# Performance work log

Measured on AMD Instinct MI355X. Metric: run time of the kernel, lower is better.

## Reference

```python
import jax, jax.numpy as jnp
import numpy as np

EPS = 1e-6
WINDOW = 1024  # config.sliding_window; mask: causal AND (q_idx - kv_idx < WINDOW)


def rms_norm(x, w=None):
    y = x * jax.lax.rsqrt(jnp.mean(jnp.square(x), axis=-1, keepdims=True) + EPS)
    return y * w if w is not None else y


def rotate_half(x):
    x1, x2 = jnp.split(x, 2, axis=-1)
    return jnp.concatenate([-x2, x1], axis=-1)


def apply_rope(x, cos, sin):
    # x: [B,S,H,D], cos/sin: [B,S,D] -> unsqueeze head dim (rotary_dim == D, x_pass empty)
    cos = cos[:, :, None, :]
    sin = sin[:, :, None, :]
    return x * cos + rotate_half(x) * sin


def setup_inputs() -> dict:
    key = jax.random.key(0)
    ks = jax.random.split(key, 8)
    B, S, HID, NH, NKV, D = 1, 2048, 2560, 8, 4, 256
    scale = 0.02
    hidden_states = jax.random.normal(ks[0], (B, S, HID), dtype=jnp.float32)
    wq = jax.random.normal(ks[1], (HID, NH * D), dtype=jnp.float32) * scale
    wk = jax.random.normal(ks[2], (HID, NKV * D), dtype=jnp.float32) * scale
    wv = jax.random.normal(ks[3], (HID, NKV * D), dtype=jnp.float32) * scale
    wo = jax.random.normal(ks[4], (NH * D, HID), dtype=jnp.float32) * scale
    q_norm_w = jnp.ones((D,), dtype=jnp.float32)
    k_norm_w = jnp.ones((D,), dtype=jnp.float32)
    # standard RoPE tables, rotary_dim = head_dim
    pos = jnp.arange(S, dtype=jnp.float32)
    inv_freq = 1.0 / (10000.0 ** (jnp.arange(0, D, 2, dtype=jnp.float32) / D))
    freqs = pos[:, None] * inv_freq[None, :]           # [S, D/2]
    emb = jnp.concatenate([freqs, freqs], axis=-1)     # [S, D]
    cos = jnp.cos(emb)[None]                           # [1, S, D]
    sin = jnp.sin(emb)[None]
    return dict(hidden_states=hidden_states, cos=cos, sin=sin,
                wq=wq, wk=wk, wv=wv, wo=wo,
                q_norm_w=q_norm_w, k_norm_w=k_norm_w)


def reference(hidden_states, cos, sin, wq, wk, wv, wo, q_norm_w, k_norm_w):
    B, S, _ = hidden_states.shape
    D = q_norm_w.shape[0]
    # projections -> [B,S,H,D]
    q = (hidden_states @ wq).reshape(B, S, -1, D)
    k = (hidden_states @ wk).reshape(B, S, -1, D)
    v = (hidden_states @ wv).reshape(B, S, -1, D)
    # QK-norm then RoPE (v gets non-affine RMSNorm)
    q = apply_rope(rms_norm(q, q_norm_w), cos, sin)
    k = apply_rope(rms_norm(k, k_norm_w), cos, sin)
    v = rms_norm(v)
    NH, NKV = q.shape[2], k.shape[2]
    rep = NH // NKV  # GQA: repeat KV heads
    k = jnp.repeat(k, rep, axis=2)
    v = jnp.repeat(v, rep, axis=2)
    # attention with scale=1.0 (QK-norm replaces 1/sqrt(d))
    scores = jnp.einsum('bqhd,bkhd->bhqk', q, k)
    qi = jnp.arange(S)[:, None]
    ki = jnp.arange(S)[None, :]
    mask = (ki <= qi) & (qi - ki < WINDOW)  # causal sliding window
    scores = jnp.where(mask[None, None], scores, -jnp.inf)
    attn = jax.nn.softmax(scores, axis=-1)
    out = jnp.einsum('bhqk,bkhd->bqhd', attn, v).reshape(B, S, -1)
    return out @ wo
```

## Files before the change

### kernel.cpp

```cpp
#include <hip/hip_runtime.h>
#include <hip/hip_bf16.h>
#include <math.h>

#define S_LEN 2048
#define HID 2560
#define NH 8
#define NKV 4
#define HD 256
#define WINDOW 1024

typedef short short8 __attribute__((ext_vector_type(8)));
typedef short short4_t __attribute__((ext_vector_type(4)));
typedef float f32x4 __attribute__((ext_vector_type(4)));
typedef float float4_t __attribute__((ext_vector_type(4)));

__device__ __forceinline__ short bf16_rne(float x) {
  unsigned u = __float_as_uint(x);
  return (short)((u + 0x7FFFu + ((u >> 16) & 1u)) >> 16);
}
__device__ __forceinline__ void split2(float x, short &h, short &l) {
  unsigned u = __float_as_uint(x);
  unsigned hb = (u + 0x7FFFu + ((u >> 16) & 1u)) & 0xFFFF0000u;
  h = (short)(hb >> 16);
  float r = x - __uint_as_float(hb);
  l = bf16_rne(r);
}

__device__ __forceinline__ void gload16(const short* g, short* l) {
  __builtin_amdgcn_global_load_lds(
      (const __attribute__((address_space(1))) void*)g,
      (__attribute__((address_space(3))) void*)l, 16, 0, 0);
}

#define SWZ(g, r) ((((g) ^ ((r) & 7))) * 8)
template <int MODE>
__device__ __forceinline__ void gemm_body(
    const short* __restrict__ Ah, const short* __restrict__ Al,
    const short* __restrict__ Bh, const short* __restrict__ Bl,
    float* __restrict__ C, int K, int ldc, int m0, int n0, int tid,
    short (*__restrict__ Ahs)[64], short (*__restrict__ Als)[64],
    short (*__restrict__ Bhs)[64], short (*__restrict__ Bls)[64]) {
  constexpr bool USE_AL = (MODE & 1) != 0;
  constexpr bool USE_BL = (MODE & 2) != 0;
  const int wv = tid >> 6, lane = tid & 63;
  const int wm = (wv >> 1) * 32, wn = (wv & 1) * 64;
  const int quad = lane >> 4, col = lane & 15;
  const int lr = lane >> 3;
  const size_t lgofs = (size_t)(((lane & 7) ^ lr)) * 8;
  const size_t aBase = (size_t)(m0 + lr) * K + lgofs;
  const size_t bBase = (size_t)(n0 + lr) * K + lgofs;

  f32x4 acc[2][4];
#pragma unroll
  for (int i = 0; i < 2; i++)
#pragma unroll
    for (int j = 0; j < 4; j++) acc[i][j] = (f32x4){0.f, 0.f, 0.f, 0.f};

  for (int k0 = 0; k0 < K; k0 += 64) {
#pragma unroll
    for (int c = wv; c < 8; c += 4) {
      const size_t go = aBase + (size_t)c * 8 * K + k0;
      gload16(Ah + go, &Ahs[c * 8][0]);
      if (USE_AL) gload16(Al + go, &Als[c * 8][0]);
    }
#pragma unroll
    for (int c = wv; c < 16; c += 4) {
      const size_t go = bBase + (size_t)c * 8 * K + k0;
      gload16(Bh + go, &Bhs[c * 8][0]);
      if (USE_BL) gload16(Bl + go, &Bls[c * 8][0]);
    }
    __syncthreads();
#pragma unroll
    for (int ks = 0; ks < 2; ks++) {
      const int g = ks * 4 + quad;
      short8 afh[2], afl[2], bfh[4], bfl[4];
#pragma unroll
      for (int i = 0; i < 2; i++) {
        int ar = wm + i * 16 + col;
        afh[i] = *reinterpret_cast<const short8*>(&Ahs[ar][SWZ(g, ar)]);
        if (USE_AL)
          afl[i] = *reinterpret_cast<const short8*>(&Als[ar][SWZ(g, ar)]);
      }
#pragma unroll
      for (int j = 0; j < 4; j++) {
        int br = wn + j * 16 + col;
        bfh[j] = *reinterpret_cast<const short8*>(&Bhs[br][SWZ(g, br)]);
        if (USE_BL)
          bfl[j] = *reinterpret_cast<const short8*>(&Bls[br][SWZ(g, br)]);
      }
#pragma unroll
      for (int i = 0; i < 2; i++)
#pragma unroll
        for (int j = 0; j < 4; j++) {
          acc[i][j] = __builtin_amdgcn_mfma_f32_16x16x32_bf16(afh[i], bfh[j], acc[i][j], 0, 0, 0);
          if (USE_BL)
            acc[i][j] = __builtin_amdgcn_mfma_f32_16x16x32_bf16(afh[i], bfl[j], acc[i][j], 0, 0, 0);
          if (USE_AL)
            acc[i][j] = __builtin_amdgcn_mfma_f32_16x16x32_bf16(afl[i], bfh[j], acc[i][j], 0, 0, 0);
        }
    }
    __syncthreads();
  }
#pragma unroll
  for (int i = 0; i < 2; i++)
#pragma unroll
    for (int j = 0; j < 4; j++)
#pragma unroll
      for (int r = 0; r < 4; r++)
        C[(size_t)(m0 + wm + i * 16 + quad * 4 + r) * ldc + n0 + wn + j * 16 + col] =
            acc[i][j][r];
}

template <int MODE>
__global__ __launch_bounds__(256, 3)
void gemm_presplit(const short* __restrict__ Ah, const short* __restrict__ Al,
                   const short* __restrict__ Bh, const short* __restrict__ Bl,
                   float* __restrict__ C, int K, int ldc) {
  __shared__ short Ahs[64][64];
  __shared__ short Als[(MODE & 1) ? 64 : 1][64];
  __shared__ short Bhs[128][64];
  __shared__ short Bls[(MODE & 2) ? 128 : 1][64];
  gemm_body<MODE>(Ah, Al, Bh, Bl, C, K, ldc, blockIdx.y * 64, blockIdx.x * 128,
                  threadIdx.x, Ahs, Als, Bhs, Bls);
}

__global__ __launch_bounds__(256, 3)
void gemm_qkv(const short* __restrict__ Ah, const short* __restrict__ Al,
              const short* __restrict__ qkvTh, const short* __restrict__ qkvTl,
              float* __restrict__ Cqkv) {
  __shared__ short Ahs[64][64];
  __shared__ short Als[64][64];
  __shared__ short Bhs[128][64];
  __shared__ short Bls[128][64];
  const int b = blockIdx.x;
  if (b < 256) {
    gemm_body<2>(Ah, Al, qkvTh + (size_t)3072 * HID, qkvTl + (size_t)3072 * HID,
                 Cqkv + 3072, HID, 4096, (b / 8) * 64, (b % 8) * 128,
                 threadIdx.x, Ahs, Als, Bhs, Bls);
  } else {
    const int t = b - 256;
    gemm_body<3>(Ah, Al, qkvTh, qkvTl, Cqkv, HID, 4096, (t / 24) * 64,
                 (t % 24) * 128, threadIdx.x, Ahs, Als, Bhs, Bls);
  }
}

__device__ __forceinline__ void wsplitT_body(const float* __restrict__ W,
                                             short* __restrict__ WTh,
                                             short* __restrict__ WTl,
                                             int KW, int NW, int n_ofs,
                                             int k0, int n0, int tid,
                                             float (*T)[65]) {
  const int r = tid >> 4, c4 = (tid & 15) * 4;
#pragma unroll
  for (int p = 0; p < 4; p++) {
    float4_t v = *reinterpret_cast<const float4_t*>(
        &W[(size_t)(k0 + r + p * 16) * NW + n0 + c4]);
#pragma unroll
    for (int e = 0; e < 4; e++) T[r + p * 16][c4 + e] = v[e];
  }
  __syncthreads();
  const int gk = tid & 7;
#pragma unroll
  for (int pass = 0; pass < 2; pass++) {
    const int n_loc = (tid >> 3) + pass * 32;
    short8 hv, lv;
#pragma unroll
    for (int e = 0; e < 8; e++) {
      short hh, ll;
      split2(T[gk * 8 + e][n_loc], hh, ll);
      hv[e] = hh; lv[e] = ll;
    }
    size_t base = (size_t)(n_ofs + n0 + n_loc) * KW + k0 + gk * 8;
    *reinterpret_cast<short8*>(WTh + base) = hv;
    *reinterpret_cast<short8*>(WTl + base) = lv;
  }
}

__global__ __launch_bounds__(256)
void prep_kernel(const float* __restrict__ hs, const float* __restrict__ wq,
                 const float* __restrict__ wk, const float* __restrict__ wv,
                 const float* __restrict__ wo, short* __restrict__ Ah,
                 short* __restrict__ Al, short* __restrict__ qkvTh,
                 short* __restrict__ qkvTl, short* __restrict__ woTh,
                 short* __restrict__ woTl) {
  __shared__ float T[64][65];
  const int bx = blockIdx.x;
  const int tid = threadIdx.x;
  if (bx < 5120) {
    const int i = bx * 256 + tid;
    float4_t v = reinterpret_cast<const float4_t*>(hs)[i];
    short4_t h, l;
#pragma unroll
    for (int e = 0; e < 4; e++) {
      short hh, ll;
      split2(v[e], hh, ll);
      h[e] = hh; l[e] = ll;
    }
    reinterpret_cast<short4_t*>(Ah)[i] = h;
    reinterpret_cast<short4_t*>(Al)[i] = l;
  } else if (bx < 6400) {
    const int local = bx - 5120;
    wsplitT_body(wq, qkvTh, qkvTl, HID, 2048, 0, (local % 40) * 64,
                 (local / 40) * 64, tid, T);
  } else if (bx < 7040) {
    const int local = bx - 6400;
    wsplitT_body(wk, qkvTh, qkvTl, HID, 1024, 2048, (local % 40) * 64,
                 (local / 40) * 64, tid, T);
  } else if (bx < 7680) {
    const int local = bx - 7040;
    wsplitT_body(wv, qkvTh, qkvTl, HID, 1024, 3072, (local % 40) * 64,
                 (local / 40) * 64, tid, T);
  } else {
    const int local = bx - 7680;
    wsplitT_body(wo, woTh, woTl, 2048, HID, 0, (local % 32) * 64,
                 (local / 32) * 64, tid, T);
  }
}

__global__ __launch_bounds__(256)
void norm_kernel(const float* __restrict__ Cqkv, const float* __restrict__ kw,
                 const float* __restrict__ cosb, const float* __restrict__ sinb,
                 short* __restrict__ kh, short* __restrict__ kl,
                 short* __restrict__ vtb) {
  const int unit = blockIdx.x * 4 + (threadIdx.x >> 6);
  const int u = unit & 7;
  const int sq = unit >> 3;
  const int t = threadIdx.x & 63;
  const int d = t * 4;
  const int colbase = (u < 4) ? 2048 + u * HD : 3072 + (u - 4) * HD;
  const float4_t x = *reinterpret_cast<const float4_t*>(
      &Cqkv[(size_t)sq * 4096 + colbase + d]);
  float v = x[0] * x[0] + x[1] * x[1] + x[2] * x[2] + x[3] * x[3];
#pragma unroll
  for (int off = 32; off; off >>= 1) v += __shfl_xor(v, off);
  const float scale = rsqrtf(v * (1.0f / HD) + 1e-6f);
  if (u < 4) {
    const float4_t w = *reinterpret_cast<const float4_t*>(kw + d);
    const float4_t cb = *reinterpret_cast<const float4_t*>(
        &cosb[(size_t)sq * HD + d]);
    const float4_t sb = *reinterpret_cast<const float4_t*>(
        &sinb[(size_t)sq * HD + d]);
    const float sgn = (t < 32) ? -1.f : 1.f;
    short4_t hv, lv;
#pragma unroll
    for (int e = 0; e < 4; e++) {
      const float n = x[e] * scale * w[e];
      const float other = __shfl_xor(n, 32);
      const float r = n * cb[e] + sgn * other * sb[e];
      short hh, ll;
      split2(r, hh, ll);
      hv[e] = hh; lv[e] = ll;
    }
    const size_t b = ((size_t)sq * NKV + u) * HD + d;
    *reinterpret_cast<short4_t*>(kh + b) = hv;
    *reinterpret_cast<short4_t*>(kl + b) = lv;
  } else {
    const int hh = u - 4;
#pragma unroll
    for (int e = 0; e < 4; e++)
      vtb[((size_t)hh * HD + d + e) * S_LEN + sq] = bf16_rne(x[e] * scale);
  }
}

#define KSW(g, r) (((g) ^ ((r) & 7)) * 8)
#define VSW(g, d) ((((g) + ((d) >> 1)) & 3) * 8)
__global__ __launch_bounds__(256, 2)
void flash_attn2(const float* __restrict__ qn, int qrs,
                 const float* __restrict__ qw, const float* __restrict__ cosb,
                 const float* __restrict__ sinb,
                 const short* __restrict__ kh, const short* __restrict__ kl,
                 const short* __restrict__ vtb, float* __restrict__ oA,
                 float* __restrict__ oB, float* __restrict__ mlA,
                 float* __restrict__ mlB) {
  __shared__ short Kh[32][256], Kl[32][256];
  __shared__ short Vb[256][32];
  __shared__ short Ps[64][32];
  const int qt = blockIdx.x, h = blockIdx.y, sp = blockIdx.z;
  const int kvh = h >> 1;
  const int q0 = qt * 64;
  const int tid = threadIdx.x;
  const int w = tid >> 6, lane = tid & 63;
  const int quad = lane >> 4, col = lane & 15;
  float* oOut = sp ? oB : oA;
  float* mlOut = sp ? mlB : mlA;
  short8 qh[8], ql[8];
  {
    const int sq = q0 + w * 16 + col;
    const float* qrow = qn + (size_t)sq * qrs + h * HD;
    float xq[8][8];
    float ssum = 0.f;
#pragma unroll
    for (int s8 = 0; s8 < 8; s8++) {
      const int d0 = s8 * 32 + quad * 8;
      float4_t a = *reinterpret_cast<const float4_t*>(qrow + d0);
      float4_t b = *reinterpret_cast<const float4_t*>(qrow + d0 + 4);
#pragma unroll
      for (int e = 0; e < 4; e++) {
        xq[s8][e] = a[e];
        xq[s8][4 + e] = b[e];
        ssum += a[e] * a[e] + b[e] * b[e];
      }
    }
    ssum += __shfl_xor(ssum, 16);
    ssum += __shfl_xor(ssum, 32);
    const float scale = rsqrtf(ssum * (1.0f / HD) + 1e-6f);
#pragma unroll
    for (int s8 = 0; s8 < 8; s8++) {
      const int d0 = s8 * 32 + quad * 8;
      float4_t w0 = *reinterpret_cast<const float4_t*>(qw + d0);
      float4_t w1 = *reinterpret_cast<const float4_t*>(qw + d0 + 4);
#pragma unroll
      for (int e = 0; e < 4; e++) {
        xq[s8][e] *= scale * w0[e];
        xq[s8][4 + e] *= scale * w1[e];
      }
    }
    const float* crow = cosb + (size_t)sq * HD;
    const float* srow = sinb + (size_t)sq * HD;
#pragma unroll
    for (int s8 = 0; s8 < 8; s8++) {
      const int d0 = s8 * 32 + quad * 8;
      float4_t c0 = *reinterpret_cast<const float4_t*>(crow + d0);
      float4_t c1 = *reinterpret_cast<const float4_t*>(crow + d0 + 4);
      float4_t s0 = *reinterpret_cast<const float4_t*>(srow + d0);
      float4_t s1 = *reinterpret_cast<const float4_t*>(srow + d0 + 4);
      const float sgn = (s8 < 4) ? -1.f : 1.f;
      const int pp = s8 ^ 4;
#pragma unroll
      for (int e = 0; e < 4; e++) {
        short hh, ll;
        split2(xq[s8][e] * c0[e] + sgn * xq[pp][e] * s0[e], hh, ll);
        qh[s8][e] = hh; ql[s8][e] = ll;
        split2(xq[s8][4 + e] * c1[e] + sgn * xq[pp][4 + e] * s1[e], hh, ll);
        qh[s8][4 + e] = hh; ql[s8][4 + e] = ll;
      }
    }
  }
  f32x4 o[16];
#pragma unroll
  for (int i = 0; i < 16; i++) o[i] = (f32x4){0.f, 0.f, 0.f, 0.f};
  float m_r[4] = {-INFINITY, -INFINITY, -INFINITY, -INFINITY};
  float l_r[4] = {0.f, 0.f, 0.f, 0.f};
  const int lo_t = (q0 > 1023) ? ((q0 - 1023) >> 5) : 0;
  const int hi_t = (q0 + 63) >> 5;
  const int halfn = (hi_t - lo_t + 2) >> 1;
  const int t0 = sp ? (lo_t + halfn) : lo_t;
  const int t1 = sp ? hi_t : (lo_t + halfn - 1);
  for (int kt = t0; kt <= t1; kt++) {
    const int kt0 = kt << 5;
    __syncthreads();
#pragma unroll
    for (int i = 0; i < 4; i++) {
      int idx = tid + i * 256;
      int row = idx >> 5, g = idx & 31;
      size_t gofs = ((size_t)(kt0 + row) * NKV + kvh) * HD + g * 8;
      *reinterpret_cast<short8*>(&Kh[row][KSW(g, row)]) =
          *reinterpret_cast<const short8*>(kh + gofs);
      *reinterpret_cast<short8*>(&Kl[row][KSW(g, row)]) =
          *reinterpret_cast<const short8*>(kl + gofs);
    }
#pragma unroll
    for (int i = 0; i < 4; i++) {
      int idx = tid + i * 256;
      int d = idx >> 2, g = idx & 3;
      *reinterpret_cast<short8*>(&Vb[d][VSW(g, d)]) =
          *reinterpret_cast<const short8*>(
              vtb + ((size_t)kvh * HD + d) * S_LEN + kt0 + g * 8);
    }
    __syncthreads();
    f32x4 sc[2];
    sc[0] = (f32x4){0.f, 0.f, 0.f, 0.f};
    sc[1] = (f32x4){0.f, 0.f, 0.f, 0.f};
#pragma unroll
    for (int s8 = 0; s8 < 8; s8++) {
#pragma unroll
      for (int nt = 0; nt < 2; nt++) {
        const int br = nt * 16 + col;
        const short8 bh = *reinterpret_cast<const short8*>(
            &Kh[br][KSW(s8 * 4 + quad, br)]);
        const short8 bl = *reinterpret_cast<const short8*>(
            &Kl[br][KSW(s8 * 4 + quad, br)]);
        sc[nt] = __builtin_amdgcn_mfma_f32_16x16x32_bf16(qh[s8], bh, sc[nt], 0, 0, 0);
        sc[nt] = __builtin_amdgcn_mfma_f32_16x16x32_bf16(qh[s8], bl, sc[nt], 0, 0, 0);
        sc[nt] = __builtin_amdgcn_mfma_f32_16x16x32_bf16(ql[s8], bh, sc[nt], 0, 0, 0);
      }
    }
#pragma unroll
    for (int r = 0; r < 4; r++) {
      const int q_abs = q0 + w * 16 + quad * 4 + r;
      const int prow = w * 16 + quad * 4 + r;
#pragma unroll
      for (int nt = 0; nt < 2; nt++) {
        int k_abs = kt0 + nt * 16 + col;
        bool valid = (k_abs <= q_abs) && (q_abs - k_abs < WINDOW);
        if (!valid) sc[nt][r] = -INFINITY;
      }
      float mx = fmaxf(sc[0][r], sc[1][r]);
      mx = fmaxf(mx, __shfl_xor(mx, 1));
      mx = fmaxf(mx, __shfl_xor(mx, 2));
      mx = fmaxf(mx, __shfl_xor(mx, 4));
      mx = fmaxf(mx, __shfl_xor(mx, 8));
      if (!__all(mx <= m_r[r] + 8.f)) {
        const float mn = fmaxf(m_r[r], mx);
        const float alpha = (mn == -INFINITY) ? 1.f : __expf(m_r[r] - mn);
        m_r[r] = mn;
        l_r[r] *= alpha;
#pragma unroll
        for (int nt2 = 0; nt2 < 16; nt2++) o[nt2][r] *= alpha;
      }
      float rsum = 0.f;
#pragma unroll
      for (int nt = 0; nt < 2; nt++) {
        float s = sc[nt][r];
        float e = (s == -INFINITY) ? 0.f : __expf(s - m_r[r]);
        rsum += e;
        int ge = nt * 2 + (col >> 3);
        Ps[prow][VSW(ge, prow) + (col & 7)] = bf16_rne(e);
      }
      rsum += __shfl_xor(rsum, 1);
      rsum += __shfl_xor(rsum, 2);
      rsum += __shfl_xor(rsum, 4);
      rsum += __shfl_xor(rsum, 8);
      l_r[r] += rsum;
    }
    __syncthreads();
    {
      const int prow = w * 16 + col;
      const short8 pa = *reinterpret_cast<const short8*>(&Ps[prow][VSW(quad, prow)]);
#pragma unroll
      for (int nt = 0; nt < 16; nt++) {
        const int vr = nt * 16 + col;
        const short8 vb = *reinterpret_cast<const short8*>(&Vb[vr][VSW(quad, vr)]);
        o[nt] = __builtin_amdgcn_mfma_f32_16x16x32_bf16(pa, vb, o[nt], 0, 0, 0);
      }
    }
  }
#pragma unroll
  for (int r = 0; r < 4; r++) {
    const int row = q0 + w * 16 + quad * 4 + r;
    const size_t base = ((size_t)row * NH + h) * HD;
#pragma unroll
    for (int nt = 0; nt < 16; nt++) oOut[base + nt * 16 + col] = o[nt][r];
    if (col == 0) {
      mlOut[((size_t)row * NH + h) * 2] = m_r[r];
      mlOut[((size_t)row * NH + h) * 2 + 1] = l_r[r];
    }
  }
}

__global__ __launch_bounds__(256)
void combine_kernel(const float* __restrict__ oA, const float* __restrict__ oB,
                    const float* __restrict__ mlA, const float* __restrict__ mlB,
                    short* __restrict__ ctxh) {
  const int idx = blockIdx.x;
  const int d = threadIdx.x;
  const float mA = mlA[(size_t)idx * 2], lA = mlA[(size_t)idx * 2 + 1];
  const float mB = mlB[(size_t)idx * 2], lB = mlB[(size_t)idx * 2 + 1];
  const float m = fmaxf(mA, mB);
  const float eA = (mA == -INFINITY) ? 0.f : __expf(mA - m);
  const float eB = (mB == -INFINITY) ? 0.f : __expf(mB - m);
  const float inv = 1.0f / (eA * lA + eB * lB);
  const size_t b = (size_t)idx * HD + d;
  ctxh[b] = bf16_rne((eA * oA[b] + eB * oB[b]) * inv);
}

extern "C" void kernel_launch(void* const* d_in, const int* in_sizes, int n_in,
                              void* d_out, int out_size, void* d_ws, size_t ws_size,
                              hipStream_t stream) {
  const float* hs   = (const float*)d_in[0];
  const float* cosb = (const float*)d_in[1];
  const float* sinb = (const float*)d_in[2];
  const float* wq   = (const float*)d_in[3];
  const float* wk   = (const float*)d_in[4];
  const float* wv   = (const float*)d_in[5];
  const float* wo   = (const float*)d_in[6];
  const float* qw   = (const float*)d_in[7];
  const float* kw   = (const float*)d_in[8];
  dim3 blk(256);

  const size_t szAh   = (size_t)S_LEN * HID * 2;
  const size_t szQKVT = (size_t)4096 * HID * 2;
  const size_t szWoT  = (size_t)HID * 2048 * 2;
  const size_t szCqkv = (size_t)S_LEN * 4096 * 4;
  const size_t szKh   = (size_t)S_LEN * NKV * HD * 2;
  const size_t szMl   = (size_t)S_LEN * NH * 2 * 4;

  char* p = (char*)d_ws + 256;
  short* Ah    = (short*)p;  p += szAh;
  short* Al    = (short*)p;  p += szAh;
  short* qkvTh = (short*)p;  p += szQKVT;
  short* qkvTl = (short*)p;  p += szQKVT;
  short* woTh  = (short*)p;  p += szWoT;
  short* woTl  = (short*)p;  p += szWoT;
  float* Cqkv  = (float*)p;  p += szCqkv;
  short* kh    = (short*)p;  p += szKh;
  short* kl    = (short*)p;  p += szKh;
  short* vtb   = (short*)p;  p += szKh;
  float* mlA   = (float*)p;  p += szMl;
  float* mlB   = (float*)p;  p += szMl;
  float* oA    = (float*)Ah;
  float* oB    = (float*)d_out;
  short* ctxh  = qkvTh;

  prep_kernel<<<8960, blk, 0, stream>>>(hs, wq, wk, wv, wo, Ah, Al, qkvTh,
                                        qkvTl, woTh, woTl);
  gemm_qkv<<<1024, blk, 0, stream>>>(Ah, Al, qkvTh, qkvTl, Cqkv);
  norm_kernel<<<4096, blk, 0, stream>>>(Cqkv, kw, cosb, sinb, kh, kl, vtb);
  flash_attn2<<<dim3(S_LEN / 64, NH, 2), blk, 0, stream>>>(
      Cqkv, 4096, qw, cosb, sinb, kh, kl, vtb, oA, oB, mlA, mlB);
  combine_kernel<<<S_LEN * NH, blk, 0, stream>>>(oA, oB, mlA, mlB, ctxh);
  gemm_presplit<2><<<dim3(HID / 128, S_LEN / 64), blk, 0, stream>>>(
      ctxh, ctxh, woTh, woTl, (float*)d_out, 2048, HID);
}
```

Baseline: 414.9 us.

## Use direct global-to-LDS loads for K/V tiles and vectorize combine kernel

```diff
diff --git a/kernel.cpp b/kernel.cpp
--- a/kernel.cpp
+++ b/kernel.cpp
@@ -283,6 +283,10 @@
   const int quad = lane >> 4, col = lane & 15;
   float* oOut = sp ? oB : oA;
   float* mlOut = sp ? mlB : mlA;
+  const int krow_lo = (lane >> 5);
+  const int ksub = 2 * w + krow_lo;
+  const int kgsrc = ((lane & 31) & 24) | ((lane & 7) ^ ksub);
+  f32x4 o[16];
   short8 qh[8], ql[8];
   {
     const int sq = q0 + w * 16 + col;
@@ -336,7 +340,6 @@
       }
     }
   }
-  f32x4 o[16];
 #pragma unroll
   for (int i = 0; i < 16; i++) o[i] = (f32x4){0.f, 0.f, 0.f, 0.f};
   float m_r[4] = {-INFINITY, -INFINITY, -INFINITY, -INFINITY};
@@ -351,21 +354,19 @@
     __syncthreads();
 #pragma unroll
     for (int i = 0; i < 4; i++) {
-      int idx = tid + i * 256;
-      int row = idx >> 5, g = idx & 31;
-      size_t gofs = ((size_t)(kt0 + row) * NKV + kvh) * HD + g * 8;
-      *reinterpret_cast<short8*>(&Kh[row][KSW(g, row)]) =
-          *reinterpret_cast<const short8*>(kh + gofs);
-      *reinterpret_cast<short8*>(&Kl[row][KSW(g, row)]) =
-          *reinterpret_cast<const short8*>(kl + gofs);
+      const int row = 8 * i + ksub;
+      const size_t gofs =
+          ((size_t)(kt0 + row) * NKV + kvh) * HD + (size_t)kgsrc * 8;
+      gload16(kh + gofs, &Kh[8 * i + 2 * w][0]);
+      gload16(kl + gofs, &Kl[8 * i + 2 * w][0]);
     }
 #pragma unroll
     for (int i = 0; i < 4; i++) {
-      int idx = tid + i * 256;
-      int d = idx >> 2, g = idx & 3;
-      *reinterpret_cast<short8*>(&Vb[d][VSW(g, d)]) =
-          *reinterpret_cast<const short8*>(
-              vtb + ((size_t)kvh * HD + d) * S_LEN + kt0 + g * 8);
+      const int d = 64 * i + 16 * w + (lane >> 2);
+      const int vgsrc = ((lane & 3) - (d >> 1)) & 3;
+      const size_t gofs =
+          ((size_t)kvh * HD + d) * S_LEN + kt0 + (size_t)vgsrc * 8;
+      gload16(vtb + gofs, &Vb[64 * i + 16 * w][0]);
     }
     __syncthreads();
     f32x4 sc[2];
@@ -452,16 +453,26 @@
 void combine_kernel(const float* __restrict__ oA, const float* __restrict__ oB,
                     const float* __restrict__ mlA, const float* __restrict__ mlB,
                     short* __restrict__ ctxh) {
-  const int idx = blockIdx.x;
-  const int d = threadIdx.x;
-  const float mA = mlA[(size_t)idx * 2], lA = mlA[(size_t)idx * 2 + 1];
-  const float mB = mlB[(size_t)idx * 2], lB = mlB[(size_t)idx * 2 + 1];
+  const int unit = blockIdx.x * 8 + (threadIdx.x >> 5);
+  const int t = threadIdx.x & 31;
+  const float mA = mlA[(size_t)unit * 2], lA = mlA[(size_t)unit * 2 + 1];
+  const float mB = mlB[(size_t)unit * 2], lB = mlB[(size_t)unit * 2 + 1];
   const float m = fmaxf(mA, mB);
   const float eA = (mA == -INFINITY) ? 0.f : __expf(mA - m);
   const float eB = (mB == -INFINITY) ? 0.f : __expf(mB - m);
   const float inv = 1.0f / (eA * lA + eB * lB);
-  const size_t b = (size_t)idx * HD + d;
-  ctxh[b] = bf16_rne((eA * oA[b] + eB * oB[b]) * inv);
+  const size_t b = (size_t)unit * HD + t * 8;
+  const float4_t a0 = *reinterpret_cast<const float4_t*>(oA + b);
+  const float4_t a1 = *reinterpret_cast<const float4_t*>(oA + b + 4);
+  const float4_t b0 = *reinterpret_cast<const float4_t*>(oB + b);
+  const float4_t b1 = *reinterpret_cast<const float4_t*>(oB + b + 4);
+  short8 out;
+#pragma unroll
+  for (int e = 0; e < 4; e++) {
+    out[e] = bf16_rne((eA * a0[e] + eB * b0[e]) * inv);
+    out[4 + e] = bf16_rne((eA * a1[e] + eB * b1[e]) * inv);
+  }
+  *reinterpret_cast<short8*>(ctxh + b) = out;
 }
 
 extern "C" void kernel_launch(void* const* d_in, const int* in_sizes, int n_in,
@@ -508,7 +519,7 @@
   norm_kernel<<<4096, blk, 0, stream>>>(Cqkv, kw, cosb, sinb, kh, kl, vtb);
   flash_attn2<<<dim3(S_LEN / 64, NH, 2), blk, 0, stream>>>(
       Cqkv, 4096, qw, cosb, sinb, kh, kl, vtb, oA, oB, mlA, mlB);
-  combine_kernel<<<S_LEN * NH, blk, 0, stream>>>(oA, oB, mlA, mlB, ctxh);
+  combine_kernel<<<2048, blk, 0, stream>>>(oA, oB, mlA, mlB, ctxh);
   gemm_presplit<2><<<dim3(HID / 128, S_LEN / 64), blk, 0, stream>>>(
       ctxh, ctxh, woTh, woTl, (float*)d_out, 2048, HID);
 }
```

After: 417.5 us. About the same (+0.6%).

## Split output GEMM along K into two halves and vectorize combine kernel

Applied to the files above, without the earlier changes.

```diff
diff --git a/kernel.cpp b/kernel.cpp
--- a/kernel.cpp
+++ b/kernel.cpp
@@ -37,7 +37,7 @@
 __device__ __forceinline__ void gemm_body(
     const short* __restrict__ Ah, const short* __restrict__ Al,
     const short* __restrict__ Bh, const short* __restrict__ Bl,
-    float* __restrict__ C, int K, int ldc, int m0, int n0, int tid,
+    float* __restrict__ C, int Klen, int Kstr, int ldc, int m0, int n0, int tid,
     short (*__restrict__ Ahs)[64], short (*__restrict__ Als)[64],
     short (*__restrict__ Bhs)[64], short (*__restrict__ Bls)[64]) {
   constexpr bool USE_AL = (MODE & 1) != 0;
@@ -47,8 +47,8 @@
   const int quad = lane >> 4, col = lane & 15;
   const int lr = lane >> 3;
   const size_t lgofs = (size_t)(((lane & 7) ^ lr)) * 8;
-  const size_t aBase = (size_t)(m0 + lr) * K + lgofs;
-  const size_t bBase = (size_t)(n0 + lr) * K + lgofs;
+  const size_t aBase = (size_t)(m0 + lr) * Kstr + lgofs;
+  const size_t bBase = (size_t)(n0 + lr) * Kstr + lgofs;
 
   f32x4 acc[2][4];
 #pragma unroll
@@ -56,16 +56,16 @@
 #pragma unroll
     for (int j = 0; j < 4; j++) acc[i][j] = (f32x4){0.f, 0.f, 0.f, 0.f};
 
-  for (int k0 = 0; k0 < K; k0 += 64) {
+  for (int k0 = 0; k0 < Klen; k0 += 64) {
 #pragma unroll
     for (int c = wv; c < 8; c += 4) {
-      const size_t go = aBase + (size_t)c * 8 * K + k0;
+      const size_t go = aBase + (size_t)c * 8 * Kstr + k0;
       gload16(Ah + go, &Ahs[c * 8][0]);
       if (USE_AL) gload16(Al + go, &Als[c * 8][0]);
     }
 #pragma unroll
     for (int c = wv; c < 16; c += 4) {
-      const size_t go = bBase + (size_t)c * 8 * K + k0;
+      const size_t go = bBase + (size_t)c * 8 * Kstr + k0;
       gload16(Bh + go, &Bhs[c * 8][0]);
       if (USE_BL) gload16(Bl + go, &Bls[c * 8][0]);
     }
@@ -109,19 +109,6 @@
       for (int r = 0; r < 4; r++)
         C[(size_t)(m0 + wm + i * 16 + quad * 4 + r) * ldc + n0 + wn + j * 16 + col] =
             acc[i][j][r];
-}
-
-template <int MODE>
-__global__ __launch_bounds__(256, 3)
-void gemm_presplit(const short* __restrict__ Ah, const short* __restrict__ Al,
-                   const short* __restrict__ Bh, const short* __restrict__ Bl,
-                   float* __restrict__ C, int K, int ldc) {
-  __shared__ short Ahs[64][64];
-  __shared__ short Als[(MODE & 1) ? 64 : 1][64];
-  __shared__ short Bhs[128][64];
-  __shared__ short Bls[(MODE & 2) ? 128 : 1][64];
-  gemm_body<MODE>(Ah, Al, Bh, Bl, C, K, ldc, blockIdx.y * 64, blockIdx.x * 128,
-                  threadIdx.x, Ahs, Als, Bhs, Bls);
 }
 
 __global__ __launch_bounds__(256, 3)
@@ -135,13 +122,46 @@
   const int b = blockIdx.x;
   if (b < 256) {
     gemm_body<2>(Ah, Al, qkvTh + (size_t)3072 * HID, qkvTl + (size_t)3072 * HID,
-                 Cqkv + 3072, HID, 4096, (b / 8) * 64, (b % 8) * 128,
+                 Cqkv + 3072, HID, HID, 4096, (b / 8) * 64, (b % 8) * 128,
                  threadIdx.x, Ahs, Als, Bhs, Bls);
   } else {
     const int t = b - 256;
-    gemm_body<3>(Ah, Al, qkvTh, qkvTl, Cqkv, HID, 4096, (t / 24) * 64,
+    gemm_body<3>(Ah, Al, qkvTh, qkvTl, Cqkv, HID, HID, 4096, (t / 24) * 64,
                  (t % 24) * 128, threadIdx.x, Ahs, Als, Bhs, Bls);
   }
+}
+
+__global__ __launch_bounds__(256, 3)
+void gemm_out(const short* __restrict__ ctxh, const short* __restrict__ woTh,
+              const short* __restrict__ woTl, float* __restrict__ C1,
+              float* __restrict__ C2) {
+  __shared__ short Ahs[64][64];
+  __shared__ short Als[1][64];
+  __shared__ short Bhs[128][64];
+  __shared__ short Bls[128][64];
+  const int b = blockIdx.x;
+  if (b < 640) {
+    gemm_body<2>(ctxh, ctxh, woTh, woTl, C1, 1024, 2048, HID,
+                 (b / 20) * 64, (b % 20) * 128, threadIdx.x, Ahs, Als, Bhs, Bls);
+  } else {
+    const int t = b - 640;
+    gemm_body<2>(ctxh + 1024, ctxh + 1024, woTh + 1024, woTl + 1024, C2, 1024,
+                 2048, HID, (t / 20) * 64, (t % 20) * 128, threadIdx.x, Ahs,
+                 Als, Bhs, Bls);
+  }
+}
+
+__global__ __launch_bounds__(256)
+void addc_kernel(float* __restrict__ dst, const float* __restrict__ src) {
+  const size_t i = ((size_t)blockIdx.x * 256 + threadIdx.x) * 2;
+  float4_t a0 = reinterpret_cast<const float4_t*>(src)[i];
+  float4_t a1 = reinterpret_cast<const float4_t*>(src)[i + 1];
+  float4_t d0 = reinterpret_cast<const float4_t*>(dst)[i];
+  float4_t d1 = reinterpret_cast<const float4_t*>(dst)[i + 1];
+#pragma unroll
+  for (int e = 0; e < 4; e++) { d0[e] += a0[e]; d1[e] += a1[e]; }
+  reinterpret_cast<float4_t*>(dst)[i] = d0;
+  reinterpret_cast<float4_t*>(dst)[i + 1] = d1;
 }
 
 __device__ __forceinline__ void wsplitT_body(const float* __restrict__ W,
@@ -452,16 +472,26 @@
 void combine_kernel(const float* __restrict__ oA, const float* __restrict__ oB,
                     const float* __restrict__ mlA, const float* __restrict__ mlB,
                     short* __restrict__ ctxh) {
-  const int idx = blockIdx.x;
-  const int d = threadIdx.x;
-  const float mA = mlA[(size_t)idx * 2], lA = mlA[(size_t)idx * 2 + 1];
-  const float mB = mlB[(size_t)idx * 2], lB = mlB[(size_t)idx * 2 + 1];
+  const int unit = blockIdx.x * 8 + (threadIdx.x >> 5);
+  const int t = threadIdx.x & 31;
+  const float mA = mlA[(size_t)unit * 2], lA = mlA[(size_t)unit * 2 + 1];
+  const float mB = mlB[(size_t)unit * 2], lB = mlB[(size_t)unit * 2 + 1];
   const float m = fmaxf(mA, mB);
   const float eA = (mA == -INFINITY) ? 0.f : __expf(mA - m);
   const float eB = (mB == -INFINITY) ? 0.f : __expf(mB - m);
   const float inv = 1.0f / (eA * lA + eB * lB);
-  const size_t b = (size_t)idx * HD + d;
-  ctxh[b] = bf16_rne((eA * oA[b] + eB * oB[b]) * inv);
+  const size_t b = (size_t)unit * HD + t * 8;
+  const float4_t a0 = *reinterpret_cast<const float4_t*>(oA + b);
+  const float4_t a1 = *reinterpret_cast<const float4_t*>(oA + b + 4);
+  const float4_t b0 = *reinterpret_cast<const float4_t*>(oB + b);
+  const float4_t b1 = *reinterpret_cast<const float4_t*>(oB + b + 4);
+  short8 out;
+#pragma unroll
+  for (int e = 0; e < 4; e++) {
+    out[e] = bf16_rne((eA * a0[e] + eB * b0[e]) * inv);
+    out[4 + e] = bf16_rne((eA * a1[e] + eB * b1[e]) * inv);
+  }
+  *reinterpret_cast<short8*>(ctxh + b) = out;
 }
 
 extern "C" void kernel_launch(void* const* d_in, const int* in_sizes, int n_in,
@@ -501,6 +531,7 @@
   float* oA    = (float*)Ah;
   float* oB    = (float*)d_out;
   short* ctxh  = qkvTh;
+  float* C2    = Cqkv;
 
   prep_kernel<<<8960, blk, 0, stream>>>(hs, wq, wk, wv, wo, Ah, Al, qkvTh,
                                         qkvTl, woTh, woTl);
@@ -508,7 +539,7 @@
   norm_kernel<<<4096, blk, 0, stream>>>(Cqkv, kw, cosb, sinb, kh, kl, vtb);
   flash_attn2<<<dim3(S_LEN / 64, NH, 2), blk, 0, stream>>>(
       Cqkv, 4096, qw, cosb, sinb, kh, kl, vtb, oA, oB, mlA, mlB);
-  combine_kernel<<<S_LEN * NH, blk, 0, stream>>>(oA, oB, mlA, mlB, ctxh);
-  gemm_presplit<2><<<dim3(HID / 128, S_LEN / 64), blk, 0, stream>>>(
-      ctxh, ctxh, woTh, woTl, (float*)d_out, 2048, HID);
-}
+  combine_kernel<<<2048, blk, 0, stream>>>(oA, oB, mlA, mlB, ctxh);
+  gemm_out<<<1280, blk, 0, stream>>>(ctxh, woTh, woTl, (float*)d_out, C2);
+  addc_kernel<<<2560, blk, 0, stream>>>((float*)d_out, C2);
+}
```

Measured after the change: 422.1 us. About the same (+1.7%).
